# Kernel tuning notes

Measured on AMD Instinct MI355X. Metric: run time of the kernel, lower is better.

## Reference

```python
import jax, jax.numpy as jnp
import numpy as np

N, DIM, NH, HD, M = 2048, 1024, 16, 64, 2
LN_EPS = 1e-5


def setup_inputs() -> dict:
    key = jax.random.key(0)
    ks = jax.random.split(key, 8)
    x = jax.random.normal(ks[0], (N, DIM), dtype=jnp.float32)
    ids = jax.random.randint(ks[1], (N,), 0, M)
    modality_masks = jnp.stack([ids == m for m in range(M)])  # [M, N] bool partition
    s = 0.02
    wq = jax.random.normal(ks[2], (M, DIM, NH * HD), dtype=jnp.float32) * s
    wk = jax.random.normal(ks[3], (M, DIM, NH * HD), dtype=jnp.float32) * s
    wv = jax.random.normal(ks[4], (M, DIM, NH * HD), dtype=jnp.float32) * s
    wo = jax.random.normal(ks[5], (M, NH * HD, DIM), dtype=jnp.float32) * s
    ln_w = jnp.ones((M, DIM), dtype=jnp.float32)
    ln_b = jnp.zeros((M, DIM), dtype=jnp.float32)
    return dict(x=x, modality_masks=modality_masks, n_heads=NH,
                wq=wq, wk=wk, wv=wv, wo=wo, ln_w=ln_w, ln_b=ln_b)


def reference(x, modality_masks, n_heads, wq, wk, wv, wo, ln_w, ln_b):
    # x: [N, dim]; modality_masks: [M, N] bool (partition of tokens)
    n_mod, n_tok = modality_masks.shape
    hd = wq.shape[-1] // n_heads
    scale = hd ** -0.5

    mod_id = jnp.argmax(modality_masks, axis=0)          # [N] modality of each token
    perm = jnp.argsort(mod_id, stable=True)              # concat order: mod-0 tokens, then mod-1, ...
    xp = x[perm]                                          # gathered tokens in expert order
    oh = jax.nn.one_hot(mod_id[perm], n_mod, dtype=x.dtype)  # [N, M] expert selector

    def expert_proj(inp, w):
        # inp: [N, din], w: [M, din, dout] -> per-token output using that token's expert
        all_out = jnp.einsum('nd,mdo->mno', inp, w)       # [M, N, dout]
        return jnp.einsum('nm,mno->no', oh, all_out)      # select expert per token

    q = expert_proj(xp, wq).reshape(n_tok, n_heads, hd).transpose(1, 0, 2)  # [H, N, hd]
    k = expert_proj(xp, wk).reshape(n_tok, n_heads, hd).transpose(1, 0, 2)
    v = expert_proj(xp, wv).reshape(n_tok, n_heads, hd).transpose(1, 0, 2)

    scores = jnp.einsum('hnd,hkd->hnk', q, k) * scale     # [H, N, N] full attention over merged tokens
    probs = jax.nn.softmax(scores, axis=-1)
    attn = jnp.einsum('hnk,hkd->hnd', probs, v)           # [H, N, hd]
    attn = attn.transpose(1, 0, 2).reshape(n_tok, n_heads * hd)

    o = expert_proj(attn, wo)                              # [N, dim] per-modality wo
    mu = jnp.mean(o, axis=-1, keepdims=True)
    var = jnp.mean((o - mu) ** 2, axis=-1, keepdims=True)
    on = (o - mu) * jax.lax.rsqrt(var + LN_EPS)
    g = oh @ ln_w                                          # [N, dim] per-token LN scale
    b = oh @ ln_b
    out_perm = on * g + b

    out = jnp.zeros_like(x).at[perm].set(out_perm)         # scatter back to original order
    return out
```

## Files before the change

### kernel.cpp

```cpp
#include <hip/hip_runtime.h>

typedef __attribute__((ext_vector_type(8))) short short8v;
typedef __attribute__((ext_vector_type(4))) float f32x4;
typedef __attribute__((ext_vector_type(16))) float f32x16;
typedef unsigned short u16;
typedef unsigned int u32;

#define MFMA __builtin_amdgcn_mfma_f32_16x16x32_bf16
#define MFMA32 __builtin_amdgcn_mfma_f32_32x32x16_bf16

__device__ __forceinline__ u16 f2b(float f) {
  u32 u = __float_as_uint(f);
  u = (u + 0x7FFFu + ((u >> 16) & 1u)) >> 16;
  return (u16)u;
}
__device__ __forceinline__ float b2f(u16 b) {
  return __uint_as_float(((u32)b) << 16);
}
__device__ __forceinline__ void g2l16(const void* g, void* l) {
  __builtin_amdgcn_global_load_lds(
      (const __attribute__((address_space(1))) unsigned int*)g,
      (__attribute__((address_space(3))) unsigned int*)l, 16, 0, 0);
}

#define N_TOK 2048
#define DIM 1024
#define NH 16
#define HD 64

#define QSCALE 0.18033688011112042f

#define OFF_PERM 0
#define OFF_CNT 8192
#define OFF_XPB 16384
#define OFF_WT (OFF_XPB + 4194304)
#define OFF_Q (OFF_WT + 16777216)
#define OFF_K (OFF_Q + 4194304)
#define OFF_V (OFF_K + 4194304)
#define OFF_VT (OFF_V + 4194304)
#define OFF_AT (OFF_VT + 4194304)
#define OFF_O (OFF_AT + 4194304)
#define OFF_O2 (OFF_O + 8388608)

__global__ __launch_bounds__(256) void prep_kernel(const void* __restrict__ masks,
                                                   int* __restrict__ perm,
                                                   int* __restrict__ cnt) {
  const int tid = threadIdx.x;
  __shared__ u32 red[256];
  __shared__ int scan[256];
  const u32* mw = (const u32*)masks;
  u32 mx = 0;
  for (int i = tid; i < 1024; i += 256) { u32 v = mw[i]; mx = mx > v ? mx : v; }
  red[tid] = mx;
  __syncthreads();
  for (int off = 128; off; off >>= 1) {
    if (tid < off) red[tid] = red[tid] > red[tid + off] ? red[tid] : red[tid + off];
    __syncthreads();
  }
  const bool isbyte = red[0] > 1u;
  int md[8];
  int c0loc = 0;
  #pragma unroll
  for (int j = 0; j < 8; ++j) {
    const int n = tid * 8 + j;
    int m1;
    if (isbyte) m1 = ((const unsigned char*)masks)[N_TOK + n] != 0;
    else        m1 = mw[N_TOK + n] != 0;
    md[j] = m1;
    c0loc += (m1 == 0);
  }
  scan[tid] = c0loc;
  __syncthreads();
  for (int off = 1; off < 256; off <<= 1) {
    int v = (tid >= off) ? scan[tid - off] : 0;
    __syncthreads();
    scan[tid] += v;
    __syncthreads();
  }
  const int incl = scan[tid];
  const int total0 = scan[255];
  const int excl0 = incl - c0loc;
  int p0 = excl0;
  int p1 = total0 + (tid * 8 - excl0);
  #pragma unroll
  for (int j = 0; j < 8; ++j) {
    const int n = tid * 8 + j;
    if (!md[j]) perm[p0++] = n; else perm[p1++] = n;
  }
  if (tid == 0) cnt[0] = total0;
}

__global__ __launch_bounds__(256) void gather_cast(const float* __restrict__ x,
                                                   const int* __restrict__ perm,
                                                   u16* __restrict__ xpb) {
  const int i = blockIdx.x;
  const int src = perm[i];
  const int tid = threadIdx.x;
  float4 v = ((const float4*)(x + (size_t)src * DIM))[tid];
  ushort4 o;
  o.x = f2b(v.x); o.y = f2b(v.y); o.z = f2b(v.z); o.w = f2b(v.w);
  ((ushort4*)(xpb + (size_t)i * DIM))[tid] = o;
}

__global__ __launch_bounds__(256) void wcast(const float* __restrict__ wq,
                                             const float* __restrict__ wk,
                                             const float* __restrict__ wv,
                                             const float* __restrict__ wo,
                                             u16* __restrict__ wT) {
  const int mat = blockIdx.z;
  const int tensor = mat >> 1, expert = mat & 1;
  const float* src = (tensor == 0) ? wq : (tensor == 1) ? wk : (tensor == 2) ? wv : wo;
  src += (size_t)expert * (1 << 20);
  u16* dst = wT + ((size_t)mat << 20);
  const int k0 = blockIdx.x * 32, n0 = blockIdx.y * 32;
  const int tx = threadIdx.x, ty = threadIdx.y;
  __shared__ float t[32][33];
  #pragma unroll
  for (int r = 0; r < 4; ++r)
    t[ty + 8 * r][tx] = src[(size_t)(k0 + ty + 8 * r) * DIM + n0 + tx];
  __syncthreads();
  #pragma unroll
  for (int r = 0; r < 4; ++r)
    dst[(size_t)(n0 + ty + 8 * r) * DIM + k0 + tx] = f2b(t[tx][ty + 8 * r]);
}

__global__ __launch_bounds__(256) void vtrans(const u16* __restrict__ v,
                                              u16* __restrict__ vT) {
  const int h = blockIdx.z;
  const int n0 = blockIdx.x * 32, d0 = blockIdx.y * 32;
  const int tx = threadIdx.x, ty = threadIdx.y;
  __shared__ u16 t[32][33];
  #pragma unroll
  for (int r = 0; r < 4; ++r)
    t[ty + 8 * r][tx] = v[(size_t)(n0 + ty + 8 * r) * DIM + h * HD + d0 + tx];
  __syncthreads();
  #pragma unroll
  for (int r = 0; r < 4; ++r)
    vT[(size_t)(h * HD + d0 + ty + 8 * r) * N_TOK + n0 + tx] = t[tx][ty + 8 * r];
}

template <int OUTF32>
__global__ __launch_bounds__(256) void gemm_exp(const u16* __restrict__ X,
                                                const u16* __restrict__ WTall,
                                                int tensor0, float scale0,
                                                int split_k,
                                                void* __restrict__ o0,
                                                void* __restrict__ o1,
                                                void* __restrict__ o2,
                                                const int* __restrict__ cntp) {
  const int z = blockIdx.z;
  const int e = blockIdx.y >> 4;
  const int mt = blockIdx.y & 15;
  const int c0 = cntp[0];
  const int lo = e ? c0 : 0;
  const int hi = e ? N_TOK : c0;
  const int rb = mt * 128;
  if (rb >= hi || rb + 128 <= lo) return;
  const int cb = blockIdx.x * 128;
  int tensor, kstart, kiters;
  void* OUT;
  float scl;
  if (split_k) {
    tensor = tensor0; OUT = z ? o1 : o0; kstart = z * 16; kiters = 16; scl = 1.f;
  } else {
    tensor = tensor0 + z; OUT = (z == 0) ? o0 : (z == 1) ? o1 : o2;
    kstart = 0; kiters = 32; scl = (z == 0) ? scale0 : 1.f;
  }
  const u16* W = WTall + ((size_t)(tensor * 2 + e) << 20);

  const int tid = threadIdx.x;
  const int w = tid >> 6, l = tid & 63, lg = l >> 4, ln = l & 15;
  const int wm = (w >> 1) * 64, wn = (w & 1) * 64;

  __shared__ __align__(16) char smem[32768];

  auto stage = [&](int it, int b_) {
    const int k0b = it * 64;
    #pragma unroll
    for (int c = 0; c < 2; ++c) {
      const int lb = (tid + c * 256) * 16;
      const int row = lb >> 6, colb = lb & 63;
      g2l16((const char*)X + (size_t)(rb + row) * 2048 + k0b + colb,
            &smem[b_ * 16384 + lb]);
      g2l16((const char*)W + (size_t)(cb + row) * 2048 + k0b + colb,
            &smem[b_ * 16384 + 8192 + lb]);
    }
  };

  f32x4 acc[4][4];
  #pragma unroll
  for (int i = 0; i < 4; ++i)
    #pragma unroll
    for (int j = 0; j < 4; ++j) acc[i][j] = (f32x4){0.f, 0.f, 0.f, 0.f};

  stage(kstart, 0);
  __syncthreads();
  for (int ii = 0; ii < kiters; ++ii) {
    const int b_ = ii & 1;
    if (ii < kiters - 1) stage(kstart + ii + 1, b_ ^ 1);
    short8v a[4], bb[4];
    #pragma unroll
    for (int mi = 0; mi < 4; ++mi)
      a[mi] = *(const short8v*)&smem[b_ * 16384 + (wm + mi * 16 + ln) * 64 + lg * 16];
    #pragma unroll
    for (int ni = 0; ni < 4; ++ni)
      bb[ni] = *(const short8v*)&smem[b_ * 16384 + 8192 + (wn + ni * 16 + ln) * 64 + lg * 16];
    __builtin_amdgcn_s_setprio(1);
    #pragma unroll
    for (int mi = 0; mi < 4; ++mi)
      #pragma unroll
      for (int ni = 0; ni < 4; ++ni)
        acc[mi][ni] = MFMA(a[mi], bb[ni], acc[mi][ni], 0, 0, 0);
    __builtin_amdgcn_s_setprio(0);
    __syncthreads();
  }

  #pragma unroll
  for (int mi = 0; mi < 4; ++mi) {
    #pragma unroll
    for (int r = 0; r < 4; ++r) {
      const int row = rb + wm + mi * 16 + lg * 4 + r;
      if (row >= lo && row < hi) {
        #pragma unroll
        for (int ni = 0; ni < 4; ++ni) {
          const int col = cb + wn + ni * 16 + ln;
          const float vv = acc[mi][ni][r] * scl;
          if (OUTF32) ((float*)OUT)[(size_t)row * DIM + col] = vv;
          else ((u16*)OUT)[(size_t)row * DIM + col] = f2b(vv);
        }
      }
    }
  }
}

__global__ __launch_bounds__(512, 4) void attn_fwd(const u16* __restrict__ qg,
                                                   const u16* __restrict__ kg,
                                                   const u16* __restrict__ vTg,
                                                   u16* __restrict__ og) {
  const int bid = blockIdx.x;
  const int wg = (bid & 7) * 64 + (bid >> 3);
  const int qt = wg & 31, h = wg >> 5;
  const int tid = threadIdx.x, w = tid >> 6, l = tid & 63;
  const int g = w & 1, kq = w >> 1;
  const int q31 = l & 31, hi = l >> 5;
  const int hi16 = hi * 16, hi4 = hi * 4;

  __shared__ __align__(16) char smem[65536];

  auto stage = [&](int it, int b_) {
    #pragma unroll
    for (int c = 0; c < 4; ++c) {
      const int j = tid + c * 512;
      const int s_ = j >> 9;
      const int rem = j & 511;
      const int isV = rem >> 8;
      const int cc = rem & 255;
      const char* src;
      if (isV) {
        const int r = cc >> 2, c16 = cc & 3;
        const int colb = (c16 * 16) ^ (((r >> 2) & 3) << 4);
        src = (const char*)vTg + (size_t)(h * HD + r) * 4096 + s_ * 1024 + it * 64 + colb;
      } else {
        const int r = cc >> 3, c16 = cc & 7;
        const int colb = (c16 * 16) ^ ((r & 7) << 4);
        src = (const char*)kg + (size_t)(s_ * 512 + it * 32 + r) * 2048 + h * 128 + colb;
      }
      g2l16(src, &smem[s_ * 16384 + b_ * 8192 + isV * 4096 + cc * 16]);
    }
  };

  const char* qrow = (const char*)qg + (size_t)(qt * 64 + g * 32 + q31) * 2048 + h * 128;
  short8v qf[4];
  #pragma unroll
  for (int t = 0; t < 4; ++t) qf[t] = *(const short8v*)(qrow + t * 32 + hi16);

  stage(0, 0);
  __syncthreads();

  float m_s = -1e30f, l_s = 0.f;
  f32x16 accO[2];
  #pragma unroll
  for (int ds = 0; ds < 2; ++ds)
    #pragma unroll
    for (int r = 0; r < 16; ++r) accO[ds][r] = 0.f;

  const int kswz = (q31 & 7) << 4;
  const int vswz = ((q31 >> 2) & 3) << 4;

  for (int it = 0; it < 16; ++it) {
    const int b_ = it & 1;
    if (it < 15) stage(it + 1, b_ ^ 1);
    const int Kb = kq * 16384 + b_ * 8192;
    const int Vb = Kb + 4096;

    short8v kf[4];
    #pragma unroll
    for (int t = 0; t < 4; ++t)
      kf[t] = *(const short8v*)&smem[Kb + q31 * 128 + ((t * 32 + hi16) ^ kswz)];
    f32x16 s_;
    #pragma unroll
    for (int r = 0; r < 16; ++r) s_[r] = 0.f;
    __builtin_amdgcn_s_setprio(1);
    s_ = MFMA32(kf[0], qf[0], s_, 0, 0, 0);
    s_ = MFMA32(kf[1], qf[1], s_, 0, 0, 0);
    s_ = MFMA32(kf[2], qf[2], s_, 0, 0, 0);
    s_ = MFMA32(kf[3], qf[3], s_, 0, 0, 0);
    __builtin_amdgcn_s_setprio(0);

    float a0 = fmaxf(fmaxf(s_[0], s_[1]), fmaxf(s_[2], s_[3]));
    float a1 = fmaxf(fmaxf(s_[4], s_[5]), fmaxf(s_[6], s_[7]));
    float a2 = fmaxf(fmaxf(s_[8], s_[9]), fmaxf(s_[10], s_[11]));
    float a3 = fmaxf(fmaxf(s_[12], s_[13]), fmaxf(s_[14], s_[15]));
    float tmax = fmaxf(fmaxf(a0, a1), fmaxf(a2, a3));
    tmax = fmaxf(tmax, __shfl_xor(tmax, 32, 64));

    if (!__all(tmax <= m_s + 11.0f)) {
      const float mn = fmaxf(m_s, tmax);
      const float al = __builtin_amdgcn_exp2f(m_s - mn);
      m_s = mn;
      l_s *= al;
      #pragma unroll
      for (int r = 0; r < 16; ++r) {
        const float ar = __shfl(al, (r & 3) + 8 * (r >> 2) + hi4, 64);
        accO[0][r] *= ar;
        accO[1][r] *= ar;
      }
    }

    float p[16];
    #pragma unroll
    for (int r = 0; r < 16; ++r) p[r] = __builtin_amdgcn_exp2f(s_[r] - m_s);
    float rs = ((p[0] + p[1]) + (p[2] + p[3])) + ((p[4] + p[5]) + (p[6] + p[7])) +
               (((p[8] + p[9]) + (p[10] + p[11])) + ((p[12] + p[13]) + (p[14] + p[15])));
    rs += __shfl_xor(rs, 32, 64);
    l_s += rs;

    u32 c0, c1, c2, c3, c4, c5, c6, c7;
    asm("v_cvt_pk_bf16_f32 %0, %1, %2" : "=v"(c0) : "v"(p[0]), "v"(p[1]));
    asm("v_cvt_pk_bf16_f32 %0, %1, %2" : "=v"(c1) : "v"(p[2]), "v"(p[3]));
    asm("v_cvt_pk_bf16_f32 %0, %1, %2" : "=v"(c2) : "v"(p[4]), "v"(p[5]));
    asm("v_cvt_pk_bf16_f32 %0, %1, %2" : "=v"(c3) : "v"(p[6]), "v"(p[7]));
    asm("v_cvt_pk_bf16_f32 %0, %1, %2" : "=v"(c4) : "v"(p[8]), "v"(p[9]));
    asm("v_cvt_pk_bf16_f32 %0, %1, %2" : "=v"(c5) : "v"(p[10]), "v"(p[11]));
    asm("v_cvt_pk_bf16_f32 %0, %1, %2" : "=v"(c6) : "v"(p[12]), "v"(p[13]));
    asm("v_cvt_pk_bf16_f32 %0, %1, %2" : "=v"(c7) : "v"(p[14]), "v"(p[15]));
    asm volatile("v_permlane32_swap_b32 %0, %1" : "+v"(c0), "+v"(c2));
    asm volatile("v_permlane32_swap_b32 %0, %1" : "+v"(c1), "+v"(c3));
    asm volatile("v_permlane32_swap_b32 %0, %1" : "+v"(c4), "+v"(c6));
    asm volatile("v_permlane32_swap_b32 %0, %1" : "+v"(c5), "+v"(c7));
    union { u32 u[4]; short8v s; } pa0, pa1;
    pa0.u[0] = c0; pa0.u[1] = c1; pa0.u[2] = c2; pa0.u[3] = c3;
    pa1.u[0] = c4; pa1.u[1] = c5; pa1.u[2] = c6; pa1.u[3] = c7;

    #pragma unroll
    for (int kst = 0; kst < 2; ++kst) {
      const short8v pa = kst ? pa1.s : pa0.s;
      short8v vb0 = *(const short8v*)&smem[Vb + q31 * 64 + ((kst * 32 + hi16) ^ vswz)];
      short8v vb1 = *(const short8v*)&smem[Vb + (32 + q31) * 64 + ((kst * 32 + hi16) ^ vswz)];
      __builtin_amdgcn_s_setprio(1);
      accO[0] = MFMA32(pa, vb0, accO[0], 0, 0, 0);
      accO[1] = MFMA32(pa, vb1, accO[1], 0, 0, 0);
      __builtin_amdgcn_s_setprio(0);
    }
    __syncthreads();
  }

  float* mm = (float*)&smem[32768];
  if (l < 32) {
    mm[(g * 4 + kq) * 32 + l] = m_s;
    mm[256 + (g * 4 + kq) * 32 + l] = l_s;
  }
  __syncthreads();
  float M = mm[(g * 4 + 0) * 32 + q31];
  M = fmaxf(M, mm[(g * 4 + 1) * 32 + q31]);
  M = fmaxf(M, mm[(g * 4 + 2) * 32 + q31]);
  M = fmaxf(M, mm[(g * 4 + 3) * 32 + q31]);
  float L = 0.f;
  #pragma unroll
  for (int j = 0; j < 4; ++j)
    L += mm[256 + (g * 4 + j) * 32 + q31] *
         __builtin_amdgcn_exp2f(mm[(g * 4 + j) * 32 + q31] - M);
  const float aown = __builtin_amdgcn_exp2f(m_s - M);
  const float linv = 1.f / L;

  float* obuf = (float*)&smem[g * 8192];
  #pragma unroll
  for (int round = 3; round >= 0; --round) {
    if (kq == round) {
      #pragma unroll
      for (int r = 0; r < 16; ++r) {
        const int qr = (r & 3) + 8 * (r >> 2) + hi4;
        const float ar = __shfl(aown, qr, 64);
        float* p0 = &obuf[qr * 64 + q31];
        float* p1 = &obuf[qr * 64 + 32 + q31];
        if (round == 3) {
          *p0 = accO[0][r] * ar;
          *p1 = accO[1][r] * ar;
        } else if (round > 0) {
          *p0 += accO[0][r] * ar;
          *p1 += accO[1][r] * ar;
        } else {
          const float li = __shfl(linv, qr, 64);
          const int row = qt * 64 + g * 32 + qr;
          og[(size_t)row * DIM + h * HD + q31] = f2b((accO[0][r] * ar + *p0) * li);
          og[(size_t)row * DIM + h * HD + 32 + q31] = f2b((accO[1][r] * ar + *p1) * li);
        }
      }
    }
    __syncthreads();
  }
}

__global__ __launch_bounds__(256) void ln_scatter(const float* __restrict__ oa,
                                                  const float* __restrict__ ob,
                                                  const float* __restrict__ lnw,
                                                  const float* __restrict__ lnb,
                                                  const int* __restrict__ perm,
                                                  const int* __restrict__ cntp,
                                                  float* __restrict__ out) {
  const int i = blockIdx.x;
  const int tid = threadIdx.x, w = tid >> 6, l = tid & 63;
  const int mod = (i < cntp[0]) ? 0 : 1;
  float4 va = ((const float4*)(oa + (size_t)i * DIM))[tid];
  float4 vb = ((const float4*)(ob + (size_t)i * DIM))[tid];
  float4 v;
  v.x = va.x + vb.x; v.y = va.y + vb.y; v.z = va.z + vb.z; v.w = va.w + vb.w;
  float s = v.x + v.y + v.z + v.w;
  float ss = v.x * v.x + v.y * v.y + v.z * v.z + v.w * v.w;
  #pragma unroll
  for (int off = 1; off < 64; off <<= 1) {
    s += __shfl_xor(s, off, 64);
    ss += __shfl_xor(ss, off, 64);
  }
  __shared__ float rs4[4], rss4[4];
  if (l == 0) { rs4[w] = s; rss4[w] = ss; }
  __syncthreads();
  const float st = rs4[0] + rs4[1] + rs4[2] + rs4[3];
  const float sst = rss4[0] + rss4[1] + rss4[2] + rss4[3];
  const float mu = st * (1.f / DIM);
  const float var = sst * (1.f / DIM) - mu * mu;
  const float rstd = rsqrtf(var + 1e-5f);
  const int drow = perm[i];
  float4 g = ((const float4*)(lnw + (size_t)mod * DIM))[tid];
  float4 b = ((const float4*)(lnb + (size_t)mod * DIM))[tid];
  float4 rr;
  rr.x = (v.x - mu) * rstd * g.x + b.x;
  rr.y = (v.y - mu) * rstd * g.y + b.y;
  rr.z = (v.z - mu) * rstd * g.z + b.z;
  rr.w = (v.w - mu) * rstd * g.w + b.w;
  ((float4*)(out + (size_t)drow * DIM))[tid] = rr;
}

extern "C" void kernel_launch(void* const* d_in, const int* in_sizes, int n_in,
                              void* d_out, int out_size, void* d_ws, size_t ws_size,
                              hipStream_t stream) {
  const float* x = (const float*)d_in[0];
  const void* masks = d_in[1];
  const float* wq = (const float*)d_in[3];
  const float* wk = (const float*)d_in[4];
  const float* wv = (const float*)d_in[5];
  const float* wo = (const float*)d_in[6];
  const float* lnw = (const float*)d_in[7];
  const float* lnb = (const float*)d_in[8];

  char* ws = (char*)d_ws;
  int* perm = (int*)(ws + OFF_PERM);
  int* cnt = (int*)(ws + OFF_CNT);
  u16* xpb = (u16*)(ws + OFF_XPB);
  u16* wT = (u16*)(ws + OFF_WT);
  u16* q = (u16*)(ws + OFF_Q);
  u16* k = (u16*)(ws + OFF_K);
  u16* v = (u16*)(ws + OFF_V);
  u16* vT = (u16*)(ws + OFF_VT);
  u16* at = (u16*)(ws + OFF_AT);
  float* o = (float*)(ws + OFF_O);
  float* o2 = (float*)(ws + OFF_O2);
  float* out = (float*)d_out;

  prep_kernel<<<1, 256, 0, stream>>>(masks, perm, cnt);
  gather_cast<<<N_TOK, 256, 0, stream>>>(x, perm, xpb);
  wcast<<<dim3(32, 32, 8), dim3(32, 8), 0, stream>>>(wq, wk, wv, wo, wT);
  gemm_exp<0><<<dim3(8, 32, 3), 256, 0, stream>>>(xpb, wT, 0, QSCALE, 0, q, k, v, cnt);
  vtrans<<<dim3(64, 2, 16), dim3(32, 8), 0, stream>>>(v, vT);
  attn_fwd<<<512, 512, 0, stream>>>(q, k, vT, at);
  gemm_exp<1><<<dim3(8, 32, 2), 256, 0, stream>>>(at, wT, 3, 1.0f, 1, o, o2, o, cnt);
  ln_scatter<<<N_TOK, 256, 0, stream>>>(o, o2, lnw, lnb, perm, cnt, out);
}
```

Measured before the change: 107.3 us.

## Fuse prep into weight cast, widen GEMM K-tile, restructure attention to register-staged KV

The mask-prep kernel is merged into the weight-cast launch as an extra z-slice, removing one launch. The expert GEMM now stages 128-wide K tiles with an XOR swizzle in 64KB of LDS, halving the iteration count and its barriers. The attention kernel moves to 256 threads where each wave processes two 32-row query groups, reusing every K/V fragment across both. K/V are prefetched through registers and written to a single LDS buffer per wave, with no per-iteration block barriers. This trades extra register pressure and lower occupancy for fewer LDS loads, fewer syncs and more MFMA work per K/V fetch.

```diff
diff --git a/kernel.cpp b/kernel.cpp
--- a/kernel.cpp
+++ b/kernel.cpp
@@ -13,9 +13,6 @@
   u32 u = __float_as_uint(f);
   u = (u + 0x7FFFu + ((u >> 16) & 1u)) >> 16;
   return (u16)u;
-}
-__device__ __forceinline__ float b2f(u16 b) {
-  return __uint_as_float(((u32)b) << 16);
 }
 __device__ __forceinline__ void g2l16(const void* g, void* l) {
   __builtin_amdgcn_global_load_lds(
@@ -42,52 +39,76 @@
 #define OFF_O (OFF_AT + 4194304)
 #define OFF_O2 (OFF_O + 8388608)
 
-__global__ __launch_bounds__(256) void prep_kernel(const void* __restrict__ masks,
-                                                   int* __restrict__ perm,
-                                                   int* __restrict__ cnt) {
-  const int tid = threadIdx.x;
+__global__ __launch_bounds__(256) void wcast_prep(const float* __restrict__ wq,
+                                                  const float* __restrict__ wk,
+                                                  const float* __restrict__ wv,
+                                                  const float* __restrict__ wo,
+                                                  u16* __restrict__ wT,
+                                                  const void* __restrict__ masks,
+                                                  int* __restrict__ perm,
+                                                  int* __restrict__ cnt) {
+  __shared__ float t[32][33];
   __shared__ u32 red[256];
   __shared__ int scan[256];
-  const u32* mw = (const u32*)masks;
-  u32 mx = 0;
-  for (int i = tid; i < 1024; i += 256) { u32 v = mw[i]; mx = mx > v ? mx : v; }
-  red[tid] = mx;
+  const int tx = threadIdx.x, ty = threadIdx.y;
+  if (blockIdx.z == 8) {
+    if (blockIdx.x != 0 || blockIdx.y != 0) return;
+    const int tid = ty * 32 + tx;
+    const u32* mw = (const u32*)masks;
+    u32 mx = 0;
+    for (int i = tid; i < 1024; i += 256) { u32 v = mw[i]; mx = mx > v ? mx : v; }
+    red[tid] = mx;
+    __syncthreads();
+    for (int off = 128; off; off >>= 1) {
+      if (tid < off) red[tid] = red[tid] > red[tid + off] ? red[tid] : red[tid + off];
+      __syncthreads();
+    }
+    const bool isbyte = red[0] > 1u;
+    int md[8];
+    int c0loc = 0;
+    #pragma unroll
+    for (int j = 0; j < 8; ++j) {
+      const int n = tid * 8 + j;
+      int m1;
+      if (isbyte) m1 = ((const unsigned char*)masks)[N_TOK + n] != 0;
+      else        m1 = mw[N_TOK + n] != 0;
+      md[j] = m1;
+      c0loc += (m1 == 0);
+    }
+    scan[tid] = c0loc;
+    __syncthreads();
+    for (int off = 1; off < 256; off <<= 1) {
+      int v = (tid >= off) ? scan[tid - off] : 0;
+      __syncthreads();
+      scan[tid] += v;
+      __syncthreads();
+    }
+    const int incl = scan[tid];
+    const int total0 = scan[255];
+    const int excl0 = incl - c0loc;
+    int p0 = excl0;
+    int p1 = total0 + (tid * 8 - excl0);
+    #pragma unroll
+    for (int j = 0; j < 8; ++j) {
+      const int n = tid * 8 + j;
+      if (!md[j]) perm[p0++] = n; else perm[p1++] = n;
+    }
+    if (tid == 0) cnt[0] = total0;
+    return;
+  }
+  const int mat = blockIdx.z;
+  const int tensor = mat >> 1, expert = mat & 1;
+  const float* src = (tensor == 0) ? wq : (tensor == 1) ? wk : (tensor == 2) ? wv : wo;
+  src += (size_t)expert * (1 << 20);
+  u16* dst = wT + ((size_t)mat << 20);
+  const int k0 = blockIdx.x * 32, n0 = blockIdx.y * 32;
+  #pragma unroll
+  for (int r = 0; r < 4; ++r)
+    t[ty + 8 * r][tx] = src[(size_t)(k0 + ty + 8 * r) * DIM + n0 + tx];
   __syncthreads();
-  for (int off = 128; off; off >>= 1) {
-    if (tid < off) red[tid] = red[tid] > red[tid + off] ? red[tid] : red[tid + off];
-    __syncthreads();
-  }
-  const bool isbyte = red[0] > 1u;
-  int md[8];
-  int c0loc = 0;
-  #pragma unroll
-  for (int j = 0; j < 8; ++j) {
-    const int n = tid * 8 + j;
-    int m1;
-    if (isbyte) m1 = ((const unsigned char*)masks)[N_TOK + n] != 0;
-    else        m1 = mw[N_TOK + n] != 0;
-    md[j] = m1;
-    c0loc += (m1 == 0);
-  }
-  scan[tid] = c0loc;
-  __syncthreads();
-  for (int off = 1; off < 256; off <<= 1) {
-    int v = (tid >= off) ? scan[tid - off] : 0;
-    __syncthreads();
-    scan[tid] += v;
-    __syncthreads();
-  }
-  const int incl = scan[tid];
-  const int total0 = scan[255];
-  const int excl0 = incl - c0loc;
-  int p0 = excl0;
-  int p1 = total0 + (tid * 8 - excl0);
-  #pragma unroll
-  for (int j = 0; j < 8; ++j) {
-    const int n = tid * 8 + j;
-    if (!md[j]) perm[p0++] = n; else perm[p1++] = n;
-  }
-  if (tid == 0) cnt[0] = total0;
+  #pragma unroll
+  for (int r = 0; r < 4; ++r)
+    dst[(size_t)(n0 + ty + 8 * r) * DIM + k0 + tx] = f2b(t[tx][ty + 8 * r]);
 }
 
 __global__ __launch_bounds__(256) void gather_cast(const float* __restrict__ x,
@@ -100,28 +121,6 @@
   ushort4 o;
   o.x = f2b(v.x); o.y = f2b(v.y); o.z = f2b(v.z); o.w = f2b(v.w);
   ((ushort4*)(xpb + (size_t)i * DIM))[tid] = o;
-}
-
-__global__ __launch_bounds__(256) void wcast(const float* __restrict__ wq,
-                                             const float* __restrict__ wk,
-                                             const float* __restrict__ wv,
-                                             const float* __restrict__ wo,
-                                             u16* __restrict__ wT) {
-  const int mat = blockIdx.z;
-  const int tensor = mat >> 1, expert = mat & 1;
-  const float* src = (tensor == 0) ? wq : (tensor == 1) ? wk : (tensor == 2) ? wv : wo;
-  src += (size_t)expert * (1 << 20);
-  u16* dst = wT + ((size_t)mat << 20);
-  const int k0 = blockIdx.x * 32, n0 = blockIdx.y * 32;
-  const int tx = threadIdx.x, ty = threadIdx.y;
-  __shared__ float t[32][33];
-  #pragma unroll
-  for (int r = 0; r < 4; ++r)
-    t[ty + 8 * r][tx] = src[(size_t)(k0 + ty + 8 * r) * DIM + n0 + tx];
-  __syncthreads();
-  #pragma unroll
-  for (int r = 0; r < 4; ++r)
-    dst[(size_t)(n0 + ty + 8 * r) * DIM + k0 + tx] = f2b(t[tx][ty + 8 * r]);
 }
 
 __global__ __launch_bounds__(256) void vtrans(const u16* __restrict__ v,
@@ -161,10 +160,10 @@
   void* OUT;
   float scl;
   if (split_k) {
-    tensor = tensor0; OUT = z ? o1 : o0; kstart = z * 16; kiters = 16; scl = 1.f;
+    tensor = tensor0; OUT = z ? o1 : o0; kstart = z * 8; kiters = 8; scl = 1.f;
   } else {
     tensor = tensor0 + z; OUT = (z == 0) ? o0 : (z == 1) ? o1 : o2;
-    kstart = 0; kiters = 32; scl = (z == 0) ? scale0 : 1.f;
+    kstart = 0; kiters = 16; scl = (z == 0) ? scale0 : 1.f;
   }
   const u16* W = WTall + ((size_t)(tensor * 2 + e) << 20);
 
@@ -172,18 +171,19 @@
   const int w = tid >> 6, l = tid & 63, lg = l >> 4, ln = l & 15;
   const int wm = (w >> 1) * 64, wn = (w & 1) * 64;
 
-  __shared__ __align__(16) char smem[32768];
+  __shared__ __align__(16) char smem[65536];
 
   auto stage = [&](int it, int b_) {
-    const int k0b = it * 64;
-    #pragma unroll
-    for (int c = 0; c < 2; ++c) {
-      const int lb = (tid + c * 256) * 16;
-      const int row = lb >> 6, colb = lb & 63;
-      g2l16((const char*)X + (size_t)(rb + row) * 2048 + k0b + colb,
-            &smem[b_ * 16384 + lb]);
-      g2l16((const char*)W + (size_t)(cb + row) * 2048 + k0b + colb,
-            &smem[b_ * 16384 + 8192 + lb]);
+    #pragma unroll
+    for (int c = 0; c < 8; ++c) {
+      const int j = tid + c * 256;
+      const int isB = j >> 10;
+      const int cc = j & 1023;
+      const int row = cc >> 3;
+      const int colb = ((cc & 7) * 16) ^ ((row & 7) << 4);
+      const char* base = isB ? (const char*)W + (size_t)(cb + row) * 2048
+                             : (const char*)X + (size_t)(rb + row) * 2048;
+      g2l16(base + it * 128 + colb, &smem[b_ * 32768 + isB * 16384 + cc * 16]);
     }
   };
 
@@ -193,25 +193,31 @@
     #pragma unroll
     for (int j = 0; j < 4; ++j) acc[i][j] = (f32x4){0.f, 0.f, 0.f, 0.f};
 
+  const int aswz = (ln & 7) << 4;
   stage(kstart, 0);
   __syncthreads();
   for (int ii = 0; ii < kiters; ++ii) {
     const int b_ = ii & 1;
     if (ii < kiters - 1) stage(kstart + ii + 1, b_ ^ 1);
-    short8v a[4], bb[4];
-    #pragma unroll
-    for (int mi = 0; mi < 4; ++mi)
-      a[mi] = *(const short8v*)&smem[b_ * 16384 + (wm + mi * 16 + ln) * 64 + lg * 16];
-    #pragma unroll
-    for (int ni = 0; ni < 4; ++ni)
-      bb[ni] = *(const short8v*)&smem[b_ * 16384 + 8192 + (wn + ni * 16 + ln) * 64 + lg * 16];
-    __builtin_amdgcn_s_setprio(1);
-    #pragma unroll
-    for (int mi = 0; mi < 4; ++mi)
+    #pragma unroll
+    for (int ks = 0; ks < 2; ++ks) {
+      short8v a[4], bb[4];
+      #pragma unroll
+      for (int mi = 0; mi < 4; ++mi)
+        a[mi] = *(const short8v*)&smem[b_ * 32768 + (wm + mi * 16 + ln) * 128 +
+                                       ((ks * 64 + lg * 16) ^ aswz)];
       #pragma unroll
       for (int ni = 0; ni < 4; ++ni)
-        acc[mi][ni] = MFMA(a[mi], bb[ni], acc[mi][ni], 0, 0, 0);
-    __builtin_amdgcn_s_setprio(0);
+        bb[ni] = *(const short8v*)&smem[b_ * 32768 + 16384 + (wn + ni * 16 + ln) * 128 +
+                                        ((ks * 64 + lg * 16) ^ aswz)];
+      __builtin_amdgcn_s_setprio(1);
+      #pragma unroll
+      for (int mi = 0; mi < 4; ++mi)
+        #pragma unroll
+        for (int ni = 0; ni < 4; ++ni)
+          acc[mi][ni] = MFMA(a[mi], bb[ni], acc[mi][ni], 0, 0, 0);
+      __builtin_amdgcn_s_setprio(0);
+    }
     __syncthreads();
   }
 
@@ -233,87 +239,75 @@
   }
 }
 
-__global__ __launch_bounds__(512, 4) void attn_fwd(const u16* __restrict__ qg,
+__global__ __launch_bounds__(256, 2) void attn_fwd(const u16* __restrict__ qg,
                                                    const u16* __restrict__ kg,
                                                    const u16* __restrict__ vTg,
                                                    u16* __restrict__ og) {
   const int bid = blockIdx.x;
   const int wg = (bid & 7) * 64 + (bid >> 3);
   const int qt = wg & 31, h = wg >> 5;
-  const int tid = threadIdx.x, w = tid >> 6, l = tid & 63;
-  const int g = w & 1, kq = w >> 1;
+  const int tid = threadIdx.x, kq = tid >> 6, l = tid & 63;
   const int q31 = l & 31, hi = l >> 5;
   const int hi16 = hi * 16, hi4 = hi * 4;
 
-  __shared__ __align__(16) char smem[65536];
-
-  auto stage = [&](int it, int b_) {
-    #pragma unroll
-    for (int c = 0; c < 4; ++c) {
-      const int j = tid + c * 512;
-      const int s_ = j >> 9;
-      const int rem = j & 511;
-      const int isV = rem >> 8;
-      const int cc = rem & 255;
-      const char* src;
-      if (isV) {
-        const int r = cc >> 2, c16 = cc & 3;
-        const int colb = (c16 * 16) ^ (((r >> 2) & 3) << 4);
-        src = (const char*)vTg + (size_t)(h * HD + r) * 4096 + s_ * 1024 + it * 64 + colb;
-      } else {
-        const int r = cc >> 3, c16 = cc & 7;
-        const int colb = (c16 * 16) ^ ((r & 7) << 4);
-        src = (const char*)kg + (size_t)(s_ * 512 + it * 32 + r) * 2048 + h * 128 + colb;
-      }
-      g2l16(src, &smem[s_ * 16384 + b_ * 8192 + isV * 4096 + cc * 16]);
-    }
+  __shared__ __align__(16) char smem[34816];
+  const int Kb = kq * 8192, Vb = Kb + 4096;
+
+  const int lr3 = l >> 3, lc3 = l & 7;
+  const char* baseK = (const char*)kg + (size_t)(kq * 512 + lr3) * 2048 + h * 128 +
+                      ((lc3 << 4) ^ (lr3 << 4));
+  const int cpr = lc3 ^ lr3;
+  const int dhalf = (cpr >> 2) & 1;
+  const char* baseV = (const char*)vTg + (size_t)(h * 64 + lr3 + dhalf * 32) * 4096 +
+                      kq * 1024 + ((cpr & 3) << 4);
+
+  const char* qb0 = (const char*)qg + (size_t)(qt * 64 + q31) * 2048 + h * 128;
+  short8v qfA[4], qfB[4];
+  #pragma unroll
+  for (int t = 0; t < 4; ++t) {
+    qfA[t] = *(const short8v*)(qb0 + t * 32 + hi16);
+    qfB[t] = *(const short8v*)(qb0 + 65536 + t * 32 + hi16);
+  }
+
+  uint4 rk0, rk1, rk2, rk3, rv0, rv1, rv2, rv3;
+  auto loadKV = [&](int it) {
+    const char* pk = baseK + (size_t)it * 65536;
+    rk0 = *(const uint4*)(pk);
+    rk1 = *(const uint4*)(pk + 16384);
+    rk2 = *(const uint4*)(pk + 32768);
+    rk3 = *(const uint4*)(pk + 49152);
+    const char* pv = baseV + it * 64;
+    rv0 = *(const uint4*)(pv);
+    rv1 = *(const uint4*)(pv + 32768);
+    rv2 = *(const uint4*)(pv + 65536);
+    rv3 = *(const uint4*)(pv + 98304);
   };
-
-  const char* qrow = (const char*)qg + (size_t)(qt * 64 + g * 32 + q31) * 2048 + h * 128;
-  short8v qf[4];
-  #pragma unroll
-  for (int t = 0; t < 4; ++t) qf[t] = *(const short8v*)(qrow + t * 32 + hi16);
-
-  stage(0, 0);
-  __syncthreads();
-
-  float m_s = -1e30f, l_s = 0.f;
-  f32x16 accO[2];
-  #pragma unroll
-  for (int ds = 0; ds < 2; ++ds)
-    #pragma unroll
-    for (int r = 0; r < 16; ++r) accO[ds][r] = 0.f;
-
-  const int kswz = (q31 & 7) << 4;
-  const int vswz = ((q31 >> 2) & 3) << 4;
-
-  for (int it = 0; it < 16; ++it) {
-    const int b_ = it & 1;
-    if (it < 15) stage(it + 1, b_ ^ 1);
-    const int Kb = kq * 16384 + b_ * 8192;
-    const int Vb = Kb + 4096;
-
-    short8v kf[4];
-    #pragma unroll
-    for (int t = 0; t < 4; ++t)
-      kf[t] = *(const short8v*)&smem[Kb + q31 * 128 + ((t * 32 + hi16) ^ kswz)];
-    f32x16 s_;
-    #pragma unroll
-    for (int r = 0; r < 16; ++r) s_[r] = 0.f;
-    __builtin_amdgcn_s_setprio(1);
-    s_ = MFMA32(kf[0], qf[0], s_, 0, 0, 0);
-    s_ = MFMA32(kf[1], qf[1], s_, 0, 0, 0);
-    s_ = MFMA32(kf[2], qf[2], s_, 0, 0, 0);
-    s_ = MFMA32(kf[3], qf[3], s_, 0, 0, 0);
-    __builtin_amdgcn_s_setprio(0);
-
-    float a0 = fmaxf(fmaxf(s_[0], s_[1]), fmaxf(s_[2], s_[3]));
-    float a1 = fmaxf(fmaxf(s_[4], s_[5]), fmaxf(s_[6], s_[7]));
-    float a2 = fmaxf(fmaxf(s_[8], s_[9]), fmaxf(s_[10], s_[11]));
-    float a3 = fmaxf(fmaxf(s_[12], s_[13]), fmaxf(s_[14], s_[15]));
-    float tmax = fmaxf(fmaxf(a0, a1), fmaxf(a2, a3));
+  auto writeK = [&]() {
+    *(uint4*)&smem[Kb + 0 + l * 16] = rk0;
+    *(uint4*)&smem[Kb + 1024 + l * 16] = rk1;
+    *(uint4*)&smem[Kb + 2048 + l * 16] = rk2;
+    *(uint4*)&smem[Kb + 3072 + l * 16] = rk3;
+  };
+  auto writeV = [&]() {
+    *(uint4*)&smem[Vb + 0 + l * 16] = rv0;
+    *(uint4*)&smem[Vb + 1024 + l * 16] = rv1;
+    *(uint4*)&smem[Vb + 2048 + l * 16] = rv2;
+    *(uint4*)&smem[Vb + 3072 + l * 16] = rv3;
+  };
+
+  float mA = -1e30f, lA = 0.f, mB = -1e30f, lB = 0.f;
+  f32x16 accA0, accA1, accB0, accB1;
+  #pragma unroll
+  for (int r = 0; r < 16; ++r) { accA0[r] = 0.f; accA1[r] = 0.f; accB0[r] = 0.f; accB1[r] = 0.f; }
+
+  struct PA { short8v p0, p1; };
+  auto softmax = [&](f32x16& s_, float& m_s, float& l_s, f32x16& a0, f32x16& a1) -> PA {
+    float t0 = fmaxf(fmaxf(s_[0], s_[1]), fmaxf(s_[2], s_[3]));
+    float t1 = fmaxf(fmaxf(s_[4], s_[5]), fmaxf(s_[6], s_[7]));
+    float t2 = fmaxf(fmaxf(s_[8], s_[9]), fmaxf(s_[10], s_[11]));
+    float t3 = fmaxf(fmaxf(s_[12], s_[13]), fmaxf(s_[14], s_[15]));
+    float tmax = fmaxf(fmaxf(t0, t1), fmaxf(t2, t3));
     tmax = fmaxf(tmax, __shfl_xor(tmax, 32, 64));
-
     if (!__all(tmax <= m_s + 11.0f)) {
       const float mn = fmaxf(m_s, tmax);
       const float al = __builtin_amdgcn_exp2f(m_s - mn);
@@ -322,11 +316,10 @@
       #pragma unroll
       for (int r = 0; r < 16; ++r) {
         const float ar = __shfl(al, (r & 3) + 8 * (r >> 2) + hi4, 64);
-        accO[0][r] *= ar;
-        accO[1][r] *= ar;
+        a0[r] *= ar;
+        a1[r] *= ar;
       }
     }
-
     float p[16];
     #pragma unroll
     for (int r = 0; r < 16; ++r) p[r] = __builtin_amdgcn_exp2f(s_[r] - m_s);
@@ -334,7 +327,6 @@
                (((p[8] + p[9]) + (p[10] + p[11])) + ((p[12] + p[13]) + (p[14] + p[15])));
     rs += __shfl_xor(rs, 32, 64);
     l_s += rs;
-
     u32 c0, c1, c2, c3, c4, c5, c6, c7;
     asm("v_cvt_pk_bf16_f32 %0, %1, %2" : "=v"(c0) : "v"(p[0]), "v"(p[1]));
     asm("v_cvt_pk_bf16_f32 %0, %1, %2" : "=v"(c1) : "v"(p[2]), "v"(p[3]));
@@ -348,62 +340,113 @@
     asm volatile("v_permlane32_swap_b32 %0, %1" : "+v"(c1), "+v"(c3));
     asm volatile("v_permlane32_swap_b32 %0, %1" : "+v"(c4), "+v"(c6));
     asm volatile("v_permlane32_swap_b32 %0, %1" : "+v"(c5), "+v"(c7));
-    union { u32 u[4]; short8v s; } pa0, pa1;
-    pa0.u[0] = c0; pa0.u[1] = c1; pa0.u[2] = c2; pa0.u[3] = c3;
-    pa1.u[0] = c4; pa1.u[1] = c5; pa1.u[2] = c6; pa1.u[3] = c7;
-
-    #pragma unroll
-    for (int kst = 0; kst < 2; ++kst) {
-      const short8v pa = kst ? pa1.s : pa0.s;
-      short8v vb0 = *(const short8v*)&smem[Vb + q31 * 64 + ((kst * 32 + hi16) ^ vswz)];
-      short8v vb1 = *(const short8v*)&smem[Vb + (32 + q31) * 64 + ((kst * 32 + hi16) ^ vswz)];
-      __builtin_amdgcn_s_setprio(1);
-      accO[0] = MFMA32(pa, vb0, accO[0], 0, 0, 0);
-      accO[1] = MFMA32(pa, vb1, accO[1], 0, 0, 0);
-      __builtin_amdgcn_s_setprio(0);
-    }
-    __syncthreads();
-  }
+    union { u32 u[4]; short8v s; } u0, u1;
+    u0.u[0] = c0; u0.u[1] = c1; u0.u[2] = c2; u0.u[3] = c3;
+    u1.u[0] = c4; u1.u[1] = c5; u1.u[2] = c6; u1.u[3] = c7;
+    PA out;
+    out.p0 = u0.s;
+    out.p1 = u1.s;
+    return out;
+  };
+
+  const int kswz = (q31 & 7) << 4;
+  loadKV(0);
+  writeK();
+  writeV();
+
+  #pragma unroll 1
+  for (int it = 0; it < 16; ++it) {
+    if (it < 15) loadKV(it + 1);
+    short8v kf0 = *(const short8v*)&smem[Kb + q31 * 128 + ((0 + hi16) ^ kswz)];
+    short8v kf1 = *(const short8v*)&smem[Kb + q31 * 128 + ((32 + hi16) ^ kswz)];
+    short8v kf2 = *(const short8v*)&smem[Kb + q31 * 128 + ((64 + hi16) ^ kswz)];
+    short8v kf3 = *(const short8v*)&smem[Kb + q31 * 128 + ((96 + hi16) ^ kswz)];
+    f32x16 sA, sB;
+    #pragma unroll
+    for (int r = 0; r < 16; ++r) { sA[r] = 0.f; sB[r] = 0.f; }
+    __builtin_amdgcn_s_setprio(1);
+    sA = MFMA32(kf0, qfA[0], sA, 0, 0, 0);
+    sB = MFMA32(kf0, qfB[0], sB, 0, 0, 0);
+    sA = MFMA32(kf1, qfA[1], sA, 0, 0, 0);
+    sB = MFMA32(kf1, qfB[1], sB, 0, 0, 0);
+    sA = MFMA32(kf2, qfA[2], sA, 0, 0, 0);
+    sB = MFMA32(kf2, qfB[2], sB, 0, 0, 0);
+    sA = MFMA32(kf3, qfA[3], sA, 0, 0, 0);
+    sB = MFMA32(kf3, qfB[3], sB, 0, 0, 0);
+    __builtin_amdgcn_s_setprio(0);
+    if (it < 15) writeK();
+
+    PA pA = softmax(sA, mA, lA, accA0, accA1);
+    PA pB = softmax(sB, mB, lB, accB0, accB1);
+
+    short8v vf00 = *(const short8v*)&smem[Vb + q31 * 128 + ((0 + hi16) ^ kswz)];
+    short8v vf01 = *(const short8v*)&smem[Vb + q31 * 128 + ((64 + hi16) ^ kswz)];
+    short8v vf10 = *(const short8v*)&smem[Vb + q31 * 128 + ((32 + hi16) ^ kswz)];
+    short8v vf11 = *(const short8v*)&smem[Vb + q31 * 128 + ((96 + hi16) ^ kswz)];
+    __builtin_amdgcn_s_setprio(1);
+    accA0 = MFMA32(pA.p0, vf00, accA0, 0, 0, 0);
+    accA1 = MFMA32(pA.p0, vf01, accA1, 0, 0, 0);
+    accB0 = MFMA32(pB.p0, vf00, accB0, 0, 0, 0);
+    accB1 = MFMA32(pB.p0, vf01, accB1, 0, 0, 0);
+    accA0 = MFMA32(pA.p1, vf10, accA0, 0, 0, 0);
+    accA1 = MFMA32(pA.p1, vf11, accA1, 0, 0, 0);
+    accB0 = MFMA32(pB.p1, vf10, accB0, 0, 0, 0);
+    accB1 = MFMA32(pB.p1, vf11, accB1, 0, 0, 0);
+    __builtin_amdgcn_s_setprio(0);
+    if (it < 15) writeV();
+  }
+  __syncthreads();
 
   float* mm = (float*)&smem[32768];
   if (l < 32) {
-    mm[(g * 4 + kq) * 32 + l] = m_s;
-    mm[256 + (g * 4 + kq) * 32 + l] = l_s;
+    mm[(0 * 4 + kq) * 32 + l] = mA;
+    mm[(1 * 4 + kq) * 32 + l] = mB;
+    mm[256 + (0 * 4 + kq) * 32 + l] = lA;
+    mm[256 + (1 * 4 + kq) * 32 + l] = lB;
   }
   __syncthreads();
-  float M = mm[(g * 4 + 0) * 32 + q31];
-  M = fmaxf(M, mm[(g * 4 + 1) * 32 + q31]);
-  M = fmaxf(M, mm[(g * 4 + 2) * 32 + q31]);
-  M = fmaxf(M, mm[(g * 4 + 3) * 32 + q31]);
-  float L = 0.f;
-  #pragma unroll
-  for (int j = 0; j < 4; ++j)
-    L += mm[256 + (g * 4 + j) * 32 + q31] *
-         __builtin_amdgcn_exp2f(mm[(g * 4 + j) * 32 + q31] - M);
-  const float aown = __builtin_amdgcn_exp2f(m_s - M);
-  const float linv = 1.f / L;
-
-  float* obuf = (float*)&smem[g * 8192];
+  float MA = mm[0 * 32 + q31], MB = mm[4 * 32 + q31];
+  #pragma unroll
+  for (int j = 1; j < 4; ++j) {
+    MA = fmaxf(MA, mm[(0 * 4 + j) * 32 + q31]);
+    MB = fmaxf(MB, mm[(1 * 4 + j) * 32 + q31]);
+  }
+  float LA = 0.f, LB = 0.f;
+  #pragma unroll
+  for (int j = 0; j < 4; ++j) {
+    LA += mm[256 + (0 * 4 + j) * 32 + q31] * __builtin_amdgcn_exp2f(mm[(0 * 4 + j) * 32 + q31] - MA);
+    LB += mm[256 + (1 * 4 + j) * 32 + q31] * __builtin_amdgcn_exp2f(mm[(1 * 4 + j) * 32 + q31] - MB);
+  }
+  const float aA = __builtin_amdgcn_exp2f(mA - MA), liA = 1.f / LA;
+  const float aB = __builtin_amdgcn_exp2f(mB - MB), liB = 1.f / LB;
+
+  float* obuf = (float*)&smem[0];
   #pragma unroll
   for (int round = 3; round >= 0; --round) {
     if (kq == round) {
       #pragma unroll
       for (int r = 0; r < 16; ++r) {
         const int qr = (r & 3) + 8 * (r >> 2) + hi4;
-        const float ar = __shfl(aown, qr, 64);
-        float* p0 = &obuf[qr * 64 + q31];
-        float* p1 = &obuf[qr * 64 + 32 + q31];
+        const float arA = __shfl(aA, qr, 64);
+        const float arB = __shfl(aB, qr, 64);
+        float* pa0 = &obuf[qr * 64 + q31];
+        float* pa1 = &obuf[qr * 64 + 32 + q31];
+        float* pb0 = &obuf[(32 + qr) * 64 + q31];
+        float* pb1 = &obuf[(32 + qr) * 64 + 32 + q31];
         if (round == 3) {
-          *p0 = accO[0][r] * ar;
-          *p1 = accO[1][r] * ar;
+          *pa0 = accA0[r] * arA; *pa1 = accA1[r] * arA;
+          *pb0 = accB0[r] * arB; *pb1 = accB1[r] * arB;
         } else if (round > 0) {
-          *p0 += accO[0][r] * ar;
-          *p1 += accO[1][r] * ar;
+          *pa0 += accA0[r] * arA; *pa1 += accA1[r] * arA;
+          *pb0 += accB0[r] * arB; *pb1 += accB1[r] * arB;
         } else {
-          const float li = __shfl(linv, qr, 64);
-          const int row = qt * 64 + g * 32 + qr;
-          og[(size_t)row * DIM + h * HD + q31] = f2b((accO[0][r] * ar + *p0) * li);
-          og[(size_t)row * DIM + h * HD + 32 + q31] = f2b((accO[1][r] * ar + *p1) * li);
+          const float lrA = __shfl(liA, qr, 64);
+          const float lrB = __shfl(liB, qr, 64);
+          const int rowA = qt * 64 + qr, rowB = qt * 64 + 32 + qr;
+          og[(size_t)rowA * DIM + h * HD + q31] = f2b((accA0[r] * arA + *pa0) * lrA);
+          og[(size_t)rowA * DIM + h * HD + 32 + q31] = f2b((accA1[r] * arA + *pa1) * lrA);
+          og[(size_t)rowB * DIM + h * HD + q31] = f2b((accB0[r] * arB + *pb0) * lrB);
+          og[(size_t)rowB * DIM + h * HD + 32 + q31] = f2b((accB1[r] * arB + *pb1) * lrB);
         }
       }
     }
@@ -477,12 +520,11 @@
   float* o2 = (float*)(ws + OFF_O2);
   float* out = (float*)d_out;
 
-  prep_kernel<<<1, 256, 0, stream>>>(masks, perm, cnt);
+  wcast_prep<<<dim3(32, 32, 9), dim3(32, 8), 0, stream>>>(wq, wk, wv, wo, wT, masks, perm, cnt);
   gather_cast<<<N_TOK, 256, 0, stream>>>(x, perm, xpb);
-  wcast<<<dim3(32, 32, 8), dim3(32, 8), 0, stream>>>(wq, wk, wv, wo, wT);
   gemm_exp<0><<<dim3(8, 32, 3), 256, 0, stream>>>(xpb, wT, 0, QSCALE, 0, q, k, v, cnt);
   vtrans<<<dim3(64, 2, 16), dim3(32, 8), 0, stream>>>(v, vT);
-  attn_fwd<<<512, 512, 0, stream>>>(q, k, vT, at);
+  attn_fwd<<<512, 256, 0, stream>>>(q, k, vT, at);
   gemm_exp<1><<<dim3(8, 32, 2), 256, 0, stream>>>(at, wT, 3, 1.0f, 1, o, o2, o, cnt);
   ln_scatter<<<N_TOK, 256, 0, stream>>>(o, o2, lnw, lnb, perm, cnt, out);
 }
```

Measured after the change: 93.75 us. 1.14x faster.
